# Kernel optimization log

Measured on AMD Instinct MI355X. Metric: run time of the kernel, lower is better.

## Reference

```python
import jax, jax.numpy as jnp
import numpy as np

# config constants
D = 1024       # main_dim
HD = 64        # attn_head_dim
NH = 16        # attention heads = D // HD
H = 16         # main_head_num (routing heads)
KH = 8         # main_key_head_num
KC = 2         # main_key_repeat_num (KH*KC == H)
N = 128        # block_size
E = 4096       # total_layer_expert_num
RE = 4         # aux_router_expert_num
DE = 4         # selected experts per router
ET = RE * DE   # 16
B, S = 1, 2048
T = B * S
BC = T // N    # 16
EPS = 1e-5
THETA = 10000.0


def rmsnorm(x, w):
    return x * jax.lax.rsqrt(jnp.mean(x * x, axis=-1, keepdims=True) + EPS) * w


def l2norm(x):
    n = jnp.sqrt(jnp.sum(x * x, axis=-1, keepdims=True))
    return x / jnp.maximum(n, EPS)


def rope(x):
    # x: (b, h, s, a); matches RotaryEmb: y1 = x1*cos + x2*sin, y2 = -x1*sin + x2*cos
    a = x.shape[-1]
    s = x.shape[2]
    inv_freq = (1.0 / THETA) ** (jnp.arange(0, a, 2, dtype=jnp.float32) / a)
    freqs = jnp.arange(s, dtype=jnp.float32)[:, None] * inv_freq[None, :]  # (s, a/2)
    cos, sin = jnp.cos(freqs), jnp.sin(freqs)
    x1, x2 = jnp.split(x, 2, axis=-1)
    return jnp.concatenate([x1 * cos + x2 * sin, -x1 * sin + x2 * cos], axis=-1)


def setup_inputs() -> dict:
    key = jax.random.key(0)
    ks = jax.random.split(key, 10)
    return {
        "x_input": jax.random.normal(ks[0], (B, S, D), jnp.float32),
        "indices": jax.random.randint(ks[1], (BC, RE, DE), 0, E),
        "scores": jax.random.normal(ks[2], (T, ET, H), jnp.float32),
        "attn_w": jax.random.normal(ks[3], (D, 3 * D), jnp.float32) * 0.02,
        "attn_out_w": jax.random.normal(ks[4], (D, D), jnp.float32) * 0.02,
        "attn_norm_w": jnp.ones((D,), jnp.float32),
        "ffn_norm_w": jnp.ones((D,), jnp.float32),
        "ffn_experts": jax.random.normal(ks[5], (3, E, D, 1), jnp.float32) * 0.02,
        "keys": jax.random.normal(ks[6], (KH, D, E), jnp.float32) * 0.02,
        "head_probs": jnp.full((1, RE, E, H), 1.0 / H, jnp.float32)
                      + 0.01 * jax.random.normal(ks[7], (1, RE, E, H), jnp.float32),
        "score_probs": jnp.full((2, 1, RE, E, H), 0.5, jnp.float32)
                       + 0.01 * jax.random.normal(ks[8], (2, 1, RE, E, H), jnp.float32),
    }


def reference(x_input, indices, scores, attn_w, attn_out_w, attn_norm_w,
              ffn_norm_w, ffn_experts, keys, head_probs, score_probs):
    # --- attention block ---
    x = rmsnorm(x_input, attn_norm_w)
    qkv = x @ attn_w                                   # (b, s, 3d)
    xq, xk, xv = jnp.split(qkv, 3, axis=-1)

    def heads(t):  # 'b s (h a) -> b h s a'
        return t.reshape(B, S, NH, HD).transpose(0, 2, 1, 3)

    xq, xk, xv = heads(xq), heads(xk), heads(xv)
    xq, xk = l2norm(xq), l2norm(xk)                    # qk_norm
    xq, xk = rope(xq), rope(xk)

    att = jnp.einsum('bhqa,bhka->bhqk', xq, xk) / np.sqrt(HD)
    causal = jnp.tril(jnp.ones((S, S), bool))
    att = jnp.where(causal, att, -jnp.inf)
    att = jax.nn.softmax(att, axis=-1)
    x_attn = jnp.einsum('bhqk,bhka->bhqa', att, xv)
    x_attn = x_attn.transpose(0, 2, 1, 3).reshape(B, S, D)
    x_attn_output = x_attn @ attn_out_w
    x_ffn_input = x_attn_output + x_input

    # --- product-key routing ---
    x_ffn = rmsnorm(x_ffn_input, ffn_norm_w)
    xf = x_ffn.reshape(T, D)

    keys_r = jnp.repeat(keys, KC, axis=0)              # (H, D, E)
    ms = jnp.einsum('td,hde->teh', xf, keys_r)         # (T, E, H)

    idx_flat = indices.reshape(BC, ET)                 # (BC, ET)
    idx_tok = jnp.repeat(idx_flat, N, axis=0)          # (T, ET), token t -> block t//N
    main_g = jnp.take_along_axis(ms, idx_tok[:, :, None], axis=1)  # (T, ET, H)

    r_idx = jnp.arange(RE)[None, :, None]
    sp = score_probs[:, 0]                             # (2, RE, E, H)
    sp_g = sp[:, r_idx, indices]                       # (2, BC, RE, DE, H)
    sp_g = jnp.repeat(sp_g.reshape(2, BC, ET, H), N, axis=1)       # (2, T, ET, H)

    comb = jax.nn.sigmoid(sp_g[0] * main_g + sp_g[1] * scores)     # (T, ET, H)

    hp_g = head_probs[0][r_idx, indices]               # (BC, RE, DE, H)
    hp_g = jnp.repeat(hp_g.reshape(BC, ET, H), N, axis=0)          # (T, ET, H)

    w = jnp.sum(comb * hp_g, axis=-1)                  # (T, ET) pair weights

    # --- grouped GEMM over tiny (d -> expert_dim -> d) experts, SwiGLU ---
    Wg = ffn_experts[:, idx_tok]                       # (3, T, ET, D, expert_dim)
    h0 = jnp.einsum('td,tedk->tek', xf, Wg[0])
    h1 = jnp.einsum('td,tedk->tek', xf, Wg[1])
    act = jax.nn.silu(h0) * h1 * w[:, :, None]         # (T, ET, expert_dim)
    out = jnp.einsum('tek,tedk->td', act, Wg[2])       # sum over selected experts

    return out.reshape(B, S, D) + x_ffn_input
```

## Files before the change

kernel.cpp:

```cpp
#include <hip/hip_runtime.h>
#include <hip/hip_bf16.h>
#include <math.h>

#define D_   1024
#define HD_  64
#define NH_  16
#define H_   16
#define KH_  8
#define NT_  128
#define E_   4096
#define RE_  4
#define DE_  4
#define ET_  16
#define S_   2048
#define T_   2048
#define BC_  16
#define EPS_ 1e-5f

typedef short s16x8 __attribute__((ext_vector_type(8)));
typedef float f32x4 __attribute__((ext_vector_type(4)));

__device__ __forceinline__ unsigned short f2bf(float f) {
    union { float f; unsigned int u; } v; v.f = f;
    unsigned int r = (v.u + 0x7fffu + ((v.u >> 16) & 1u)) >> 16;
    return (unsigned short)r;
}

#define GLOAD16(gp, lp) __builtin_amdgcn_global_load_lds(                      \
    (__attribute__((address_space(1))) void*)(gp),                             \
    (__attribute__((address_space(3))) void*)(lp), 16, 0, 0)

__global__ __launch_bounds__(256) void preprocess_kernel(
    const float* __restrict__ x, const float* __restrict__ attn_norm_w,
    unsigned short* __restrict__ xnb,
    const float* __restrict__ attn_w, unsigned short* __restrict__ wqkvT,
    const float* __restrict__ attn_out_w, unsigned short* __restrict__ woutT,
    const float* __restrict__ keys, const int* __restrict__ indices,
    unsigned short* __restrict__ kgath)
{
    __shared__ float tile[32][33];
    __shared__ float sred[4];
    int bid = blockIdx.x, tid = threadIdx.x;

    if (bid < 2048) {
        int row = bid;
        float4 v = ((const float4*)(x + (size_t)row * D_))[tid];
        float ss = v.x*v.x + v.y*v.y + v.z*v.z + v.w*v.w;
#pragma unroll
        for (int off = 32; off > 0; off >>= 1) ss += __shfl_xor(ss, off);
        if ((tid & 63) == 0) sred[tid >> 6] = ss;
        __syncthreads();
        float tot = sred[0] + sred[1] + sred[2] + sred[3];
        float scale = rsqrtf(tot * (1.0f / D_) + EPS_);
        float4 wv = ((const float4*)attn_norm_w)[tid];
        ushort4 o;
        o.x = f2bf(v.x * scale * wv.x);
        o.y = f2bf(v.y * scale * wv.y);
        o.z = f2bf(v.z * scale * wv.z);
        o.w = f2bf(v.w * scale * wv.w);
        *(ushort4*)(xnb + (size_t)row * D_ + tid * 4) = o;
    } else if (bid < 6144) {
        const float* src; unsigned short* dst; int R, Ncols, bx, by;
        if (bid < 5120) {
            int cid = bid - 2048;
            src = attn_w; dst = wqkvT; R = D_; Ncols = 3 * D_;
            bx = (cid % 96) * 32; by = (cid / 96) * 32;
        } else {
            int cid = bid - 5120;
            src = attn_out_w; dst = woutT; R = D_; Ncols = D_;
            bx = (cid & 31) * 32; by = (cid >> 5) * 32;
        }
        int tx = tid & 31, ty = tid >> 5;
#pragma unroll
        for (int rr = 0; rr < 32; rr += 8)
            tile[ty + rr][tx] = src[(size_t)(by + ty + rr) * Ncols + bx + tx];
        __syncthreads();
#pragma unroll
        for (int rr = 0; rr < 32; rr += 8)
            dst[(size_t)(bx + ty + rr) * R + by + tx] = f2bf(tile[tx][ty + rr]);
    } else {
        int gid = bid - 6144;
        int pair = gid >> 3, kh = gid & 7;
        int idx = indices[pair];
        const float* kp = keys + (size_t)kh * D_ * E_ + idx;
        int d = tid * 4;
        ushort4 o;
        o.x = f2bf(kp[(size_t)(d + 0) * E_]);
        o.y = f2bf(kp[(size_t)(d + 1) * E_]);
        o.z = f2bf(kp[(size_t)(d + 2) * E_]);
        o.w = f2bf(kp[(size_t)(d + 3) * E_]);
        *(ushort4*)(kgath + ((size_t)pair * KH_ + kh) * D_ + d) = o;
    }
}

__global__ __launch_bounds__(256) void rmsnorm_dual_kernel(
    const float* __restrict__ x, const float* __restrict__ w,
    float* __restrict__ out, unsigned short* __restrict__ outb)
{
    int row = blockIdx.x, tid = threadIdx.x;
    __shared__ float sred[4];
    float4 v = ((const float4*)(x + (size_t)row * D_))[tid];
    float ss = v.x*v.x + v.y*v.y + v.z*v.z + v.w*v.w;
#pragma unroll
    for (int off = 32; off > 0; off >>= 1) ss += __shfl_xor(ss, off);
    if ((tid & 63) == 0) sred[tid >> 6] = ss;
    __syncthreads();
    float tot = sred[0] + sred[1] + sred[2] + sred[3];
    float scale = rsqrtf(tot * (1.0f / D_) + EPS_);
    float4 wv = ((const float4*)w)[tid];
    float4 o;
    o.x = v.x * scale * wv.x;
    o.y = v.y * scale * wv.y;
    o.z = v.z * scale * wv.z;
    o.w = v.w * scale * wv.w;
    ((float4*)(out + (size_t)row * D_))[tid] = o;
    ushort4 ob;
    ob.x = f2bf(o.x); ob.y = f2bf(o.y); ob.z = f2bf(o.z); ob.w = f2bf(o.w);
    *(ushort4*)(outb + (size_t)row * D_ + tid * 4) = ob;
}

__global__ __launch_bounds__(256) void transpose_v_kernel(
    const unsigned short* __restrict__ src, unsigned short* __restrict__ dst)
{
    __shared__ unsigned short tile[32][34];
    int h  = blockIdx.z;
    int d0 = blockIdx.x * 32;
    int s0 = blockIdx.y * 32;
    int tx = threadIdx.x & 31, ty = threadIdx.x >> 5;
    const unsigned short* sp = src + ((size_t)h * S_ + s0) * HD_ + d0;
#pragma unroll
    for (int rr = 0; rr < 32; rr += 8)
        tile[ty + rr][tx] = sp[(size_t)(ty + rr) * HD_ + tx];
    __syncthreads();
    unsigned short* dp = dst + ((size_t)h * HD_ + d0) * S_ + s0;
#pragma unroll
    for (int rr = 0; rr < 32; rr += 8)
        dp[(size_t)(ty + rr) * S_ + tx] = tile[tx][ty + rr];
}

template <int WITH_RES>
__global__ __launch_bounds__(256) void mfma_gemm_kernel(
    const unsigned short* __restrict__ A, const unsigned short* __restrict__ Bt,
    const float* __restrict__ res, float* __restrict__ C,
    int M, int N, int K)
{
    __shared__ __align__(16) short As[128][32];
    __shared__ __align__(16) short Bs[128][32];
    int tid = threadIdx.x;
    int wave = tid >> 6, lane = tid & 63;
    int ml = lane & 15, q = lane >> 4;
    int wr = wave >> 1, wc = wave & 1;
    int bm = blockIdx.y * 128, bn = blockIdx.x * 128;
    int srow = tid >> 2;
    int scol = (tid & 3) * 8;

    f32x4 acc[4][4];
#pragma unroll
    for (int i = 0; i < 4; i++)
#pragma unroll
        for (int j = 0; j < 4; j++) acc[i][j] = (f32x4){0.f, 0.f, 0.f, 0.f};

    const unsigned short* Ap = A  + (size_t)(bm + srow) * K + scol;
    const unsigned short* Bp = Bt + (size_t)(bn + srow) * K + scol;
    short* ldsA0 = &As[wave * 16][0];
    short* ldsA1 = &As[64 + wave * 16][0];
    short* ldsB0 = &Bs[wave * 16][0];
    short* ldsB1 = &Bs[64 + wave * 16][0];

    for (int k0 = 0; k0 < K; k0 += 32) {
        __syncthreads();
        GLOAD16(Ap + k0, ldsA0);
        GLOAD16(Ap + (size_t)64 * K + k0, ldsA1);
        GLOAD16(Bp + k0, ldsB0);
        GLOAD16(Bp + (size_t)64 * K + k0, ldsB1);
        __syncthreads();

        s16x8 af[4], bf[4];
#pragma unroll
        for (int i = 0; i < 4; i++)
            af[i] = *(const s16x8*)(&As[wr * 64 + i * 16 + ml][q * 8]);
#pragma unroll
        for (int j = 0; j < 4; j++)
            bf[j] = *(const s16x8*)(&Bs[wc * 64 + j * 16 + ml][q * 8]);
#pragma unroll
        for (int i = 0; i < 4; i++)
#pragma unroll
            for (int j = 0; j < 4; j++)
                acc[i][j] = __builtin_amdgcn_mfma_f32_16x16x32_bf16(
                    af[i], bf[j], acc[i][j], 0, 0, 0);
    }

#pragma unroll
    for (int i = 0; i < 4; i++) {
#pragma unroll
        for (int j = 0; j < 4; j++) {
            int col = bn + wc * 64 + j * 16 + ml;
#pragma unroll
            for (int r = 0; r < 4; r++) {
                int row = bm + wr * 64 + i * 16 + q * 4 + r;
                float v = acc[i][j][r];
                if (WITH_RES) v += res[(size_t)row * N + col];
                C[(size_t)row * N + col] = v;
            }
        }
    }
}

__global__ __launch_bounds__(256) void mfma_gemm_qkv_kernel(
    const unsigned short* __restrict__ A, const unsigned short* __restrict__ Bt,
    unsigned short* __restrict__ qh, unsigned short* __restrict__ khb,
    unsigned short* __restrict__ vhb)
{
    const int K = D_;
    __shared__ __align__(16) short As[128][32];
    __shared__ __align__(16) short Bs[128][32];
    int tid = threadIdx.x;
    int wave = tid >> 6, lane = tid & 63;
    int ml = lane & 15, q = lane >> 4;
    int wr = wave >> 1, wc = wave & 1;
    int bm = blockIdx.y * 128, bn = blockIdx.x * 128;
    int srow = tid >> 2;
    int scol = (tid & 3) * 8;

    f32x4 acc[4][4];
#pragma unroll
    for (int i = 0; i < 4; i++)
#pragma unroll
        for (int j = 0; j < 4; j++) acc[i][j] = (f32x4){0.f, 0.f, 0.f, 0.f};

    const unsigned short* Ap = A  + (size_t)(bm + srow) * K + scol;
    const unsigned short* Bp = Bt + (size_t)(bn + srow) * K + scol;
    short* ldsA0 = &As[wave * 16][0];
    short* ldsA1 = &As[64 + wave * 16][0];
    short* ldsB0 = &Bs[wave * 16][0];
    short* ldsB1 = &Bs[64 + wave * 16][0];

    for (int k0 = 0; k0 < K; k0 += 32) {
        __syncthreads();
        GLOAD16(Ap + k0, ldsA0);
        GLOAD16(Ap + (size_t)64 * K + k0, ldsA1);
        GLOAD16(Bp + k0, ldsB0);
        GLOAD16(Bp + (size_t)64 * K + k0, ldsB1);
        __syncthreads();

        s16x8 af[4], bf[4];
#pragma unroll
        for (int i = 0; i < 4; i++)
            af[i] = *(const s16x8*)(&As[wr * 64 + i * 16 + ml][q * 8]);
#pragma unroll
        for (int j = 0; j < 4; j++)
            bf[j] = *(const s16x8*)(&Bs[wc * 64 + j * 16 + ml][q * 8]);
#pragma unroll
        for (int i = 0; i < 4; i++)
#pragma unroll
            for (int j = 0; j < 4; j++)
                acc[i][j] = __builtin_amdgcn_mfma_f32_16x16x32_bf16(
                    af[i], bf[j], acc[i][j], 0, 0, 0);
    }

    int sel = blockIdx.x >> 3;
    int h = ((blockIdx.x & 7) << 1) + wc;
    unsigned short* dst = (sel == 0) ? qh : (sel == 1) ? khb : vhb;
    float qscale = (sel == 0) ? 0.125f : 1.0f;
    float if0 = exp2f((float)ml * (-13.287712379549449f / 32.0f));
    float if1 = exp2f((float)(16 + ml) * (-13.287712379549449f / 32.0f));

#pragma unroll
    for (int i = 0; i < 4; i++) {
#pragma unroll
        for (int r = 0; r < 4; r++) {
            int row = bm + wr * 64 + i * 16 + q * 4 + r;
            float v0 = acc[i][0][r], v1 = acc[i][1][r];
            float v2 = acc[i][2][r], v3 = acc[i][3][r];
            if (sel < 2) {
                float ss = v0*v0 + v1*v1 + v2*v2 + v3*v3;
#pragma unroll
                for (int off = 1; off < 16; off <<= 1)
                    ss += __shfl_xor(ss, off);
                float inv = qscale / fmaxf(sqrtf(ss), EPS_);
                v0 *= inv; v1 *= inv; v2 *= inv; v3 *= inv;
                float sn0, cs0, sn1, cs1;
                sincosf((float)row * if0, &sn0, &cs0);
                sincosf((float)row * if1, &sn1, &cs1);
                float o0 = v0 * cs0 + v2 * sn0;
                float o2 = v2 * cs0 - v0 * sn0;
                float o1 = v1 * cs1 + v3 * sn1;
                float o3 = v3 * cs1 - v1 * sn1;
                v0 = o0; v1 = o1; v2 = o2; v3 = o3;
            }
            size_t base = ((size_t)h * S_ + row) * HD_;
            dst[base +      ml] = f2bf(v0);
            dst[base + 16 + ml] = f2bf(v1);
            dst[base + 32 + ml] = f2bf(v2);
            dst[base + 48 + ml] = f2bf(v3);
        }
    }
}

#define FS 72
__global__ __launch_bounds__(256) void flash_attn_mfma_kernel(
    const unsigned short* __restrict__ qh, const unsigned short* __restrict__ khb,
    const unsigned short* __restrict__ vhT, unsigned short* __restrict__ aob)
{
    __shared__ __align__(16) short Ks[2][64][FS];
    __shared__ __align__(16) short Vs[2][64][FS];
    __shared__ __align__(16) short Ps[4][16][FS];
    int u = blockIdx.x & 255;
    int v = blockIdx.x >> 8;
    int h = u & 15;
    int p = u >> 4;
    int t = v ? (31 - p) : p;
    int tid = threadIdx.x;
    int wq = tid >> 6;
    int lane = tid & 63;
    int ml = lane & 15, quad = lane >> 4;
    int srow = tid >> 2;
    int sc = (tid & 3) * 16;
    const unsigned short* Qb = qh  + (size_t)h * S_ * HD_;
    const unsigned short* Kb = khb + (size_t)h * S_ * HD_;
    const unsigned short* Vt = vhT + (size_t)h * HD_ * S_;

    int q0 = t * 64;
    int qrow = q0 + wq * 16 + ml;
    s16x8 aq0 = *(const s16x8*)(Qb + (size_t)qrow * HD_ + quad * 8);
    s16x8 aq1 = *(const s16x8*)(Qb + (size_t)qrow * HD_ + 32 + quad * 8);

    float m[4], l[4];
    f32x4 o[4];
#pragma unroll
    for (int r = 0; r < 4; r++) { m[r] = -INFINITY; l[r] = 0.f; }
#pragma unroll
    for (int nb = 0; nb < 4; nb++) o[nb] = (f32x4){0.f, 0.f, 0.f, 0.f};

    int4 kr0, kr1, vr0, vr1;
    {
        const unsigned short* kp = Kb + (size_t)srow * HD_ + sc;
        kr0 = *(const int4*)kp; kr1 = *(const int4*)(kp + 8);
        const unsigned short* vp = Vt + (size_t)srow * S_ + sc;
        vr0 = *(const int4*)vp; vr1 = *(const int4*)(vp + 8);
        *(int4*)(&Ks[0][srow][sc]) = kr0; *(int4*)(&Ks[0][srow][sc + 8]) = kr1;
        *(int4*)(&Vs[0][srow][sc]) = vr0; *(int4*)(&Vs[0][srow][sc + 8]) = vr1;
    }
    __syncthreads();
    int cur = 0;

    for (int kt = 0; kt <= t; kt++) {
        int k0 = kt * 64;
        if (kt < t) {
            const unsigned short* kp = Kb + (size_t)(k0 + 64 + srow) * HD_ + sc;
            kr0 = *(const int4*)kp; kr1 = *(const int4*)(kp + 8);
            const unsigned short* vp = Vt + (size_t)srow * S_ + k0 + 64 + sc;
            vr0 = *(const int4*)vp; vr1 = *(const int4*)(vp + 8);
        }

        f32x4 s[4];
#pragma unroll
        for (int nb = 0; nb < 4; nb++) s[nb] = (f32x4){0.f, 0.f, 0.f, 0.f};
        __builtin_amdgcn_s_setprio(1);
#pragma unroll
        for (int nb = 0; nb < 4; nb++) {
            s16x8 b0 = *(const s16x8*)(&Ks[cur][nb * 16 + ml][quad * 8]);
            s16x8 b1 = *(const s16x8*)(&Ks[cur][nb * 16 + ml][32 + quad * 8]);
            s[nb] = __builtin_amdgcn_mfma_f32_16x16x32_bf16(aq0, b0, s[nb], 0, 0, 0);
            s[nb] = __builtin_amdgcn_mfma_f32_16x16x32_bf16(aq1, b1, s[nb], 0, 0, 0);
        }
        __builtin_amdgcn_s_setprio(0);

        float sv[4][4];
#pragma unroll
        for (int nb = 0; nb < 4; nb++)
#pragma unroll
            for (int r = 0; r < 4; r++) {
                float val = s[nb][r];
                if (kt == t && (nb * 16 + ml) > (wq * 16 + quad * 4 + r))
                    val = -1e30f;
                sv[nb][r] = val;
            }
#pragma unroll
        for (int r = 0; r < 4; r++) {
            float rm = fmaxf(fmaxf(sv[0][r], sv[1][r]),
                             fmaxf(sv[2][r], sv[3][r]));
#pragma unroll
            for (int off = 1; off < 16; off <<= 1)
                rm = fmaxf(rm, __shfl_xor(rm, off));
            float mn = fmaxf(m[r], rm);
            float corr = __expf(m[r] - mn);
            m[r] = mn;
            float rs = 0.f;
#pragma unroll
            for (int nb = 0; nb < 4; nb++) {
                float pe = __expf(sv[nb][r] - mn);
                sv[nb][r] = pe;
                rs += pe;
            }
#pragma unroll
            for (int off = 1; off < 16; off <<= 1)
                rs += __shfl_xor(rs, off);
            l[r] = l[r] * corr + rs;
#pragma unroll
            for (int nb = 0; nb < 4; nb++) o[nb][r] *= corr;
        }

#pragma unroll
        for (int nb = 0; nb < 4; nb++)
#pragma unroll
            for (int r = 0; r < 4; r++)
                Ps[wq][quad * 4 + r][nb * 16 + ml] = (short)f2bf(sv[nb][r]);

        s16x8 ap0 = *(const s16x8*)(&Ps[wq][ml][quad * 8]);
        s16x8 ap1 = *(const s16x8*)(&Ps[wq][ml][32 + quad * 8]);
        __builtin_amdgcn_s_setprio(1);
#pragma unroll
        for (int nb = 0; nb < 4; nb++) {
            s16x8 b0 = *(const s16x8*)(&Vs[cur][nb * 16 + ml][quad * 8]);
            s16x8 b1 = *(const s16x8*)(&Vs[cur][nb * 16 + ml][32 + quad * 8]);
            o[nb] = __builtin_amdgcn_mfma_f32_16x16x32_bf16(ap0, b0, o[nb], 0, 0, 0);
            o[nb] = __builtin_amdgcn_mfma_f32_16x16x32_bf16(ap1, b1, o[nb], 0, 0, 0);
        }
        __builtin_amdgcn_s_setprio(0);

        __syncthreads();
        if (kt < t) {
            *(int4*)(&Ks[cur ^ 1][srow][sc])     = kr0;
            *(int4*)(&Ks[cur ^ 1][srow][sc + 8]) = kr1;
            *(int4*)(&Vs[cur ^ 1][srow][sc])     = vr0;
            *(int4*)(&Vs[cur ^ 1][srow][sc + 8]) = vr1;
            __syncthreads();
            cur ^= 1;
        }
    }

#pragma unroll
    for (int r = 0; r < 4; r++) {
        float inv = 1.0f / l[r];
        int row = q0 + wq * 16 + quad * 4 + r;
#pragma unroll
        for (int nb = 0; nb < 4; nb++)
            aob[(size_t)row * D_ + h * HD_ + nb * 16 + ml] =
                f2bf(o[nb][r] * inv);
    }
}

__global__ __launch_bounds__(256) void score_gemm_kernel(
    const unsigned short* __restrict__ xfb, const unsigned short* __restrict__ kgath,
    float* __restrict__ msbufp)
{
    __shared__ __align__(16) short As[128][32];
    __shared__ __align__(16) short Bs[128][32];
    int c  = blockIdx.x >> 3;
    int sk = blockIdx.x & 7;
    const unsigned short* A  = xfb   + (size_t)c * 128 * D_ + sk * 128;
    const unsigned short* Bt = kgath + (size_t)c * 128 * D_ + sk * 128;
    int tid = threadIdx.x;
    int wave = tid >> 6, lane = tid & 63;
    int ml = lane & 15, q = lane >> 4;
    int wr = wave >> 1, wc = wave & 1;
    int srow = tid >> 2;
    int scol = (tid & 3) * 8;

    f32x4 acc[4][4];
#pragma unroll
    for (int i = 0; i < 4; i++)
#pragma unroll
        for (int j = 0; j < 4; j++) acc[i][j] = (f32x4){0.f, 0.f, 0.f, 0.f};

    const unsigned short* Ap = A  + (size_t)srow * D_ + scol;
    const unsigned short* Bp = Bt + (size_t)srow * D_ + scol;
    short* ldsA0 = &As[wave * 16][0];
    short* ldsA1 = &As[64 + wave * 16][0];
    short* ldsB0 = &Bs[wave * 16][0];
    short* ldsB1 = &Bs[64 + wave * 16][0];

    for (int k0 = 0; k0 < 128; k0 += 32) {
        __syncthreads();
        GLOAD16(Ap + k0, ldsA0);
        GLOAD16(Ap + (size_t)64 * D_ + k0, ldsA1);
        GLOAD16(Bp + k0, ldsB0);
        GLOAD16(Bp + (size_t)64 * D_ + k0, ldsB1);
        __syncthreads();

        s16x8 af[4], bf[4];
#pragma unroll
        for (int i = 0; i < 4; i++)
            af[i] = *(const s16x8*)(&As[wr * 64 + i * 16 + ml][q * 8]);
#pragma unroll
        for (int j = 0; j < 4; j++)
            bf[j] = *(const s16x8*)(&Bs[wc * 64 + j * 16 + ml][q * 8]);
#pragma unroll
        for (int i = 0; i < 4; i++)
#pragma unroll
            for (int j = 0; j < 4; j++)
                acc[i][j] = __builtin_amdgcn_mfma_f32_16x16x32_bf16(
                    af[i], bf[j], acc[i][j], 0, 0, 0);
    }

    float* out = msbufp + (size_t)blockIdx.x * 128 * 128;
#pragma unroll
    for (int i = 0; i < 4; i++)
#pragma unroll
        for (int j = 0; j < 4; j++) {
            int col = wc * 64 + j * 16 + ml;
#pragma unroll
            for (int r = 0; r < 4; r++) {
                int row = wr * 64 + i * 16 + q * 4 + r;
                out[(size_t)row * 128 + col] = acc[i][j][r];
            }
        }
}

__global__ __launch_bounds__(256) void moe_kernel(
    const float* __restrict__ xf, const float* __restrict__ xfi,
    const int* __restrict__ indices, const float* __restrict__ msbufp,
    const float* __restrict__ scores,
    const float* __restrict__ score_probs, const float* __restrict__ head_probs,
    const float* __restrict__ experts, float* __restrict__ out)
{
    int t = blockIdx.x, tid = threadIdx.x;
    int c = t >> 7;
    int trow = t & 127;
    __shared__ int sidx[ET_];
    __shared__ float sw[ET_];
    __shared__ float sact[ET_];
    __shared__ float sx[D_];
    if (tid < ET_) sidx[tid] = indices[c * ET_ + tid];
    float4 xv = ((const float4*)(xf + (size_t)t * D_))[tid];
    ((float4*)sx)[tid] = xv;
    {
        int e = tid >> 4, hh = tid & 15;
        int idx = indices[c * ET_ + e];
        int rr = e >> 2;
        const float* mp = msbufp + ((size_t)(c * 8) * 128 + trow) * 128
                                 + e * 8 + (hh >> 1);
        float ms = 0.f;
#pragma unroll
        for (int sck = 0; sck < 8; sck++) ms += mp[(size_t)sck * 128 * 128];
        float scv = scores[(size_t)t * (ET_ * H_) + tid];
        float sp0 = score_probs[((size_t)rr * E_ + idx) * H_ + hh];
        float sp1 = score_probs[((size_t)(RE_ + rr) * E_ + idx) * H_ + hh];
        float hp  = head_probs[((size_t)rr * E_ + idx) * H_ + hh];
        float z = sp0 * ms + sp1 * scv;
        float term = hp / (1.0f + __expf(-z));
#pragma unroll
        for (int off = 1; off < 16; off <<= 1)
            term += __shfl_xor(term, off);
        if (hh == 0) sw[e] = term;
    }
    __syncthreads();

    int wv = tid >> 6, lane = tid & 63;
#pragma unroll
    for (int ee = 0; ee < 4; ee++) {
        int e = wv * 4 + ee;
        int idx = sidx[e];
        size_t base = (size_t)idx * D_;
        float p0 = 0.f, p1 = 0.f;
#pragma unroll
        for (int rr = 0; rr < 4; rr++) {
            int dd = rr * 256 + lane * 4;
            float4 xr = *(const float4*)(sx + dd);
            float4 w0 = *(const float4*)(experts + base + dd);
            float4 w1 = *(const float4*)(experts + (size_t)E_ * D_ + base + dd);
            p0 += xr.x*w0.x + xr.y*w0.y + xr.z*w0.z + xr.w*w0.w;
            p1 += xr.x*w1.x + xr.y*w1.y + xr.z*w1.z + xr.w*w1.w;
        }
#pragma unroll
        for (int off = 32; off > 0; off >>= 1) {
            p0 += __shfl_xor(p0, off);
            p1 += __shfl_xor(p1, off);
        }
        if (lane == 0)
            sact[e] = p0 / (1.0f + __expf(-p0)) * p1 * sw[e];
    }
    __syncthreads();

    float a0 = 0.f, a1 = 0.f, a2 = 0.f, a3 = 0.f;
    const float* w2base = experts + (size_t)2 * E_ * D_;
#pragma unroll
    for (int e = 0; e < ET_; e++) {
        float act = sact[e];
        float4 w2 = *(const float4*)(w2base + (size_t)sidx[e] * D_ + tid * 4);
        a0 += act * w2.x;
        a1 += act * w2.y;
        a2 += act * w2.z;
        a3 += act * w2.w;
    }
    size_t o = (size_t)t * D_ + tid * 4;
    float4 rv = *(const float4*)(xfi + o);
    float4 ov;
    ov.x = a0 + rv.x;
    ov.y = a1 + rv.y;
    ov.z = a2 + rv.z;
    ov.w = a3 + rv.w;
    *(float4*)(out + o) = ov;
}

extern "C" void kernel_launch(void* const* d_in, const int* in_sizes, int n_in,
                              void* d_out, int out_size, void* d_ws, size_t ws_size,
                              hipStream_t stream)
{
    (void)in_sizes; (void)n_in; (void)out_size; (void)ws_size;
    const float* x_input     = (const float*)d_in[0];
    const int*   indices     = (const int*)d_in[1];
    const float* scores      = (const float*)d_in[2];
    const float* attn_w      = (const float*)d_in[3];
    const float* attn_out_w  = (const float*)d_in[4];
    const float* attn_norm_w = (const float*)d_in[5];
    const float* ffn_norm_w  = (const float*)d_in[6];
    const float* ffn_experts = (const float*)d_in[7];
    const float* keys        = (const float*)d_in[8];
    const float* head_probs  = (const float*)d_in[9];
    const float* score_probs = (const float*)d_in[10];
    float* out = (float*)d_out;

    float* ws = (float*)d_ws;
    const size_t MF = 1024 * 1024;
    unsigned short* qh    = (unsigned short*)ws;
    unsigned short* khb   = (unsigned short*)(ws + 1 * MF);
    unsigned short* vhb   = (unsigned short*)(ws + 2 * MF);
    unsigned short* vhT   = (unsigned short*)(ws + 3 * MF);
    float* xfi            = ws + 4 * MF;
    unsigned short* xnb   = (unsigned short*)(ws + 6 * MF);
    unsigned short* aob   = (unsigned short*)(ws + 6 * MF);
    unsigned short* woutT = (unsigned short*)(ws + 7 * MF);
    unsigned short* wqkvT = (unsigned short*)(ws + 8 * MF);
    float* xf             = ws + 8 * MF;
    unsigned short* kgath = (unsigned short*)(ws + 10 * MF);
    unsigned short* xfb   = (unsigned short*)(ws + 11 * MF);
    float* msbufp         = ws + 12 * MF;

    preprocess_kernel<<<8192, 256, 0, stream>>>(
        x_input, attn_norm_w, xnb, attn_w, wqkvT, attn_out_w, woutT,
        keys, indices, kgath);

    {
        dim3 g(3 * D_ / 128, T_ / 128);
        mfma_gemm_qkv_kernel<<<g, 256, 0, stream>>>(xnb, wqkvT, qh, khb, vhb);
    }

    {
        dim3 g(HD_ / 32, S_ / 32, NH_);
        transpose_v_kernel<<<g, 256, 0, stream>>>(vhb, vhT);
    }

    flash_attn_mfma_kernel<<<(S_ / 64) * NH_, 256, 0, stream>>>(qh, khb, vhT, aob);

    {
        dim3 g(D_ / 128, T_ / 128);
        mfma_gemm_kernel<1><<<g, 256, 0, stream>>>(aob, woutT, x_input, xfi,
                                                   T_, D_, D_);
    }

    rmsnorm_dual_kernel<<<T_, 256, 0, stream>>>(xfi, ffn_norm_w, xf, xfb);

    score_gemm_kernel<<<BC_ * 8, 256, 0, stream>>>(xfb, kgath, msbufp);

    moe_kernel<<<T_, 256, 0, stream>>>(xf, xfi, indices, msbufp, scores,
                                       score_probs, head_probs,
                                       ffn_experts, out);
}
```

Measured before the change: 396.9 us.

## Drop online-softmax max tracking and batch four tokens per MoE block

```diff
diff --git a/kernel.cpp b/kernel.cpp
--- a/kernel.cpp
+++ b/kernel.cpp
@@ -325,10 +325,10 @@
     s16x8 aq0 = *(const s16x8*)(Qb + (size_t)qrow * HD_ + quad * 8);
     s16x8 aq1 = *(const s16x8*)(Qb + (size_t)qrow * HD_ + 32 + quad * 8);
 
-    float m[4], l[4];
+    float ps[4];
     f32x4 o[4];
 #pragma unroll
-    for (int r = 0; r < 4; r++) { m[r] = -INFINITY; l[r] = 0.f; }
+    for (int r = 0; r < 4; r++) ps[r] = 0.f;
 #pragma unroll
     for (int nb = 0; nb < 4; nb++) o[nb] = (f32x4){0.f, 0.f, 0.f, 0.f};
 
@@ -366,46 +366,16 @@
         }
         __builtin_amdgcn_s_setprio(0);
 
-        float sv[4][4];
 #pragma unroll
         for (int nb = 0; nb < 4; nb++)
 #pragma unroll
             for (int r = 0; r < 4; r++) {
-                float val = s[nb][r];
+                float pe = __expf(s[nb][r]);
                 if (kt == t && (nb * 16 + ml) > (wq * 16 + quad * 4 + r))
-                    val = -1e30f;
-                sv[nb][r] = val;
+                    pe = 0.f;
+                ps[r] += pe;
+                Ps[wq][quad * 4 + r][nb * 16 + ml] = (short)f2bf(pe);
             }
-#pragma unroll
-        for (int r = 0; r < 4; r++) {
-            float rm = fmaxf(fmaxf(sv[0][r], sv[1][r]),
-                             fmaxf(sv[2][r], sv[3][r]));
-#pragma unroll
-            for (int off = 1; off < 16; off <<= 1)
-                rm = fmaxf(rm, __shfl_xor(rm, off));
-            float mn = fmaxf(m[r], rm);
-            float corr = __expf(m[r] - mn);
-            m[r] = mn;
-            float rs = 0.f;
-#pragma unroll
-            for (int nb = 0; nb < 4; nb++) {
-                float pe = __expf(sv[nb][r] - mn);
-                sv[nb][r] = pe;
-                rs += pe;
-            }
-#pragma unroll
-            for (int off = 1; off < 16; off <<= 1)
-                rs += __shfl_xor(rs, off);
-            l[r] = l[r] * corr + rs;
-#pragma unroll
-            for (int nb = 0; nb < 4; nb++) o[nb][r] *= corr;
-        }
-
-#pragma unroll
-        for (int nb = 0; nb < 4; nb++)
-#pragma unroll
-            for (int r = 0; r < 4; r++)
-                Ps[wq][quad * 4 + r][nb * 16 + ml] = (short)f2bf(sv[nb][r]);
 
         s16x8 ap0 = *(const s16x8*)(&Ps[wq][ml][quad * 8]);
         s16x8 ap1 = *(const s16x8*)(&Ps[wq][ml][32 + quad * 8]);
@@ -432,7 +402,11 @@
 
 #pragma unroll
     for (int r = 0; r < 4; r++) {
-        float inv = 1.0f / l[r];
+        float l = ps[r];
+#pragma unroll
+        for (int off = 1; off < 16; off <<= 1)
+            l += __shfl_xor(l, off);
+        float inv = 1.0f / l;
         int row = q0 + wq * 16 + quad * 4 + r;
 #pragma unroll
         for (int nb = 0; nb < 4; nb++)
@@ -515,35 +489,43 @@
     const float* __restrict__ score_probs, const float* __restrict__ head_probs,
     const float* __restrict__ experts, float* __restrict__ out)
 {
-    int t = blockIdx.x, tid = threadIdx.x;
-    int c = t >> 7;
-    int trow = t & 127;
+    int g = blockIdx.x, tid = threadIdx.x;
+    int c = g >> 5;
+    int t0 = c * NT_ + (g & 31) * 4;
     __shared__ int sidx[ET_];
-    __shared__ float sw[ET_];
-    __shared__ float sact[ET_];
-    __shared__ float sx[D_];
+    __shared__ float sw[4][ET_];
+    __shared__ float sact[4][ET_];
+    __shared__ float sx[4][D_];
     if (tid < ET_) sidx[tid] = indices[c * ET_ + tid];
-    float4 xv = ((const float4*)(xf + (size_t)t * D_))[tid];
-    ((float4*)sx)[tid] = xv;
+#pragma unroll
+    for (int tt = 0; tt < 4; tt++)
+        ((float4*)sx[tt])[tid] =
+            ((const float4*)(xf + (size_t)(t0 + tt) * D_))[tid];
     {
         int e = tid >> 4, hh = tid & 15;
-        int idx = indices[c * ET_ + e];
+        int idxe = indices[c * ET_ + e];
         int rr = e >> 2;
-        const float* mp = msbufp + ((size_t)(c * 8) * 128 + trow) * 128
-                                 + e * 8 + (hh >> 1);
-        float ms = 0.f;
-#pragma unroll
-        for (int sck = 0; sck < 8; sck++) ms += mp[(size_t)sck * 128 * 128];
-        float scv = scores[(size_t)t * (ET_ * H_) + tid];
-        float sp0 = score_probs[((size_t)rr * E_ + idx) * H_ + hh];
-        float sp1 = score_probs[((size_t)(RE_ + rr) * E_ + idx) * H_ + hh];
-        float hp  = head_probs[((size_t)rr * E_ + idx) * H_ + hh];
-        float z = sp0 * ms + sp1 * scv;
-        float term = hp / (1.0f + __expf(-z));
-#pragma unroll
-        for (int off = 1; off < 16; off <<= 1)
-            term += __shfl_xor(term, off);
-        if (hh == 0) sw[e] = term;
+        float sp0 = score_probs[((size_t)rr * E_ + idxe) * H_ + hh];
+        float sp1 = score_probs[((size_t)(RE_ + rr) * E_ + idxe) * H_ + hh];
+        float hp  = head_probs[((size_t)rr * E_ + idxe) * H_ + hh];
+#pragma unroll
+        for (int tt = 0; tt < 4; tt++) {
+            int t = t0 + tt;
+            int trow = t & 127;
+            const float* mp = msbufp + ((size_t)(c * 8) * 128 + trow) * 128
+                                     + e * 8 + (hh >> 1);
+            float ms = 0.f;
+#pragma unroll
+            for (int sck = 0; sck < 8; sck++)
+                ms += mp[(size_t)sck * 128 * 128];
+            float scv = scores[(size_t)t * (ET_ * H_) + tid];
+            float z = sp0 * ms + sp1 * scv;
+            float term = hp / (1.0f + __expf(-z));
+#pragma unroll
+            for (int off = 1; off < 16; off <<= 1)
+                term += __shfl_xor(term, off);
+            if (hh == 0) sw[tt][e] = term;
+        }
     }
     __syncthreads();
 
@@ -553,45 +535,60 @@
         int e = wv * 4 + ee;
         int idx = sidx[e];
         size_t base = (size_t)idx * D_;
-        float p0 = 0.f, p1 = 0.f;
+        float p0[4] = {0.f, 0.f, 0.f, 0.f};
+        float p1[4] = {0.f, 0.f, 0.f, 0.f};
 #pragma unroll
         for (int rr = 0; rr < 4; rr++) {
             int dd = rr * 256 + lane * 4;
-            float4 xr = *(const float4*)(sx + dd);
             float4 w0 = *(const float4*)(experts + base + dd);
             float4 w1 = *(const float4*)(experts + (size_t)E_ * D_ + base + dd);
-            p0 += xr.x*w0.x + xr.y*w0.y + xr.z*w0.z + xr.w*w0.w;
-            p1 += xr.x*w1.x + xr.y*w1.y + xr.z*w1.z + xr.w*w1.w;
-        }
-#pragma unroll
-        for (int off = 32; off > 0; off >>= 1) {
-            p0 += __shfl_xor(p0, off);
-            p1 += __shfl_xor(p1, off);
-        }
-        if (lane == 0)
-            sact[e] = p0 / (1.0f + __expf(-p0)) * p1 * sw[e];
+#pragma unroll
+            for (int tt = 0; tt < 4; tt++) {
+                float4 xr = *(const float4*)(&sx[tt][dd]);
+                p0[tt] += xr.x*w0.x + xr.y*w0.y + xr.z*w0.z + xr.w*w0.w;
+                p1[tt] += xr.x*w1.x + xr.y*w1.y + xr.z*w1.z + xr.w*w1.w;
+            }
+        }
+#pragma unroll
+        for (int tt = 0; tt < 4; tt++) {
+#pragma unroll
+            for (int off = 32; off > 0; off >>= 1) {
+                p0[tt] += __shfl_xor(p0[tt], off);
+                p1[tt] += __shfl_xor(p1[tt], off);
+            }
+        }
+        if (lane == 0) {
+#pragma unroll
+            for (int tt = 0; tt < 4; tt++)
+                sact[tt][e] = p0[tt] / (1.0f + __expf(-p0[tt])) * p1[tt]
+                              * sw[tt][e];
+        }
     }
     __syncthreads();
 
-    float a0 = 0.f, a1 = 0.f, a2 = 0.f, a3 = 0.f;
+    float4 a0 = {0,0,0,0}, a1 = {0,0,0,0}, a2 = {0,0,0,0}, a3 = {0,0,0,0};
     const float* w2base = experts + (size_t)2 * E_ * D_;
 #pragma unroll
     for (int e = 0; e < ET_; e++) {
-        float act = sact[e];
         float4 w2 = *(const float4*)(w2base + (size_t)sidx[e] * D_ + tid * 4);
-        a0 += act * w2.x;
-        a1 += act * w2.y;
-        a2 += act * w2.z;
-        a3 += act * w2.w;
-    }
-    size_t o = (size_t)t * D_ + tid * 4;
-    float4 rv = *(const float4*)(xfi + o);
-    float4 ov;
-    ov.x = a0 + rv.x;
-    ov.y = a1 + rv.y;
-    ov.z = a2 + rv.z;
-    ov.w = a3 + rv.w;
-    *(float4*)(out + o) = ov;
+        float c0 = sact[0][e], c1 = sact[1][e], c2 = sact[2][e], c3 = sact[3][e];
+        a0.x += c0 * w2.x; a0.y += c0 * w2.y; a0.z += c0 * w2.z; a0.w += c0 * w2.w;
+        a1.x += c1 * w2.x; a1.y += c1 * w2.y; a1.z += c1 * w2.z; a1.w += c1 * w2.w;
+        a2.x += c2 * w2.x; a2.y += c2 * w2.y; a2.z += c2 * w2.z; a2.w += c2 * w2.w;
+        a3.x += c3 * w2.x; a3.y += c3 * w2.y; a3.z += c3 * w2.z; a3.w += c3 * w2.w;
+    }
+#pragma unroll
+    for (int tt = 0; tt < 4; tt++) {
+        float4 av = (tt == 0) ? a0 : (tt == 1) ? a1 : (tt == 2) ? a2 : a3;
+        size_t o = (size_t)(t0 + tt) * D_ + tid * 4;
+        float4 rv = *(const float4*)(xfi + o);
+        float4 ov;
+        ov.x = av.x + rv.x;
+        ov.y = av.y + rv.y;
+        ov.z = av.z + rv.z;
+        ov.w = av.w + rv.w;
+        *(float4*)(out + o) = ov;
+    }
 }
 
 extern "C" void kernel_launch(void* const* d_in, const int* in_sizes, int n_in,
@@ -654,7 +651,7 @@
 
     score_gemm_kernel<<<BC_ * 8, 256, 0, stream>>>(xfb, kgath, msbufp);
 
-    moe_kernel<<<T_, 256, 0, stream>>>(xf, xfi, indices, msbufp, scores,
-                                       score_probs, head_probs,
-                                       ffn_experts, out);
-}
+    moe_kernel<<<T_ / 4, 256, 0, stream>>>(xf, xfi, indices, msbufp, scores,
+                                           score_probs, head_probs,
+                                           ffn_experts, out);
+}
```

Measured after the change: 375.7 us. 1.06x faster.
